# Kernel optimization log

Hardware: AMD Instinct MI355X
Metric: run time of the kernel (lower is better)

## Reference

```python
import jax, jax.numpy as jnp
import numpy as np


def setup_inputs() -> dict:
    key = jax.random.key(0)
    k1, k2, k3 = jax.random.split(key, 3)
    B, S, H, E = 4, 4096, 7168, 256
    return {
        "hidden_states": jax.random.normal(k1, (B, S, H), dtype=jnp.float32),
        "gate_weight": jax.random.normal(k2, (E, H), dtype=jnp.float32) * (H ** -0.5),
        "bias": jax.random.normal(k3, (E,), dtype=jnp.float32) * 0.01,
        "n_group": 8,
        "topk_group": 4,
        "top_k": 8,
    }


def reference(hidden_states, gate_weight, bias, n_group, topk_group, top_k):
    B, S, H = hidden_states.shape
    E = gate_weight.shape[0]
    group_size = E // n_group
    x = hidden_states.reshape(-1, H)  # [T, H]
    logits = jnp.einsum("th,eh->te", x, gate_weight)  # [T, E]
    scores = jax.nn.sigmoid(logits) + bias  # [T, E]
    scores_g = scores.reshape(-1, n_group, group_size)  # [T, G, E/G]
    group_scores = scores_g.max(axis=-1)  # [T, G]
    _, sel_groups = jax.lax.top_k(group_scores, topk_group)  # [T, topk_group]
    # group mask: 1.0 for selected groups (indices are distinct, so sum of one-hots is 0/1)
    group_mask = jax.nn.one_hot(sel_groups, n_group, dtype=scores.dtype).sum(axis=1)  # [T, G]
    masked = (scores_g * group_mask[:, :, None]).reshape(-1, E)  # [T, E]
    weights, indices = jax.lax.top_k(masked, top_k)  # [T, top_k]
    weights = weights / (weights.sum(axis=-1, keepdims=True) + 1e-6)
    return weights.reshape(B, S, -1), indices.reshape(B, S, -1)
```

## Files before the change

kernel.cpp:

```cpp
#include <hip/hip_runtime.h>


#define TTOK 16384
#define EEXP 256
#define HDIM 7168
#define BM 128
#define BK 64
#define SPLITK 2
#define KSLICE (HDIM / SPLITK)
#define NSTEP (KSLICE / BK)
#define NTHR 512
#define LDS_BYTES 163840
#define ABASE 131072
#define EPI_LDS (64 * 257 * 4)

typedef __attribute__((ext_vector_type(4))) float f32x4;
typedef __attribute__((ext_vector_type(8))) _Float16 h8;

__device__ __forceinline__ void gload_lds16(const void* g, void* l) {
  typedef const __attribute__((address_space(1))) unsigned int gu32;
  typedef __attribute__((address_space(3))) unsigned int lu32;
  __builtin_amdgcn_global_load_lds((gu32*)g, (lu32*)l, 16, 0, 0);
}

__global__ __launch_bounds__(64) void pack_w_kernel(const float* __restrict__ W,
                                                    _Float16* __restrict__ blob) {
  const int kcg = blockIdx.x;
  const int eb = blockIdx.y;
  const int lane = threadIdx.x;
  const int e = eb * 16 + (lane & 15);
  const int k0 = kcg * 32 + (lane >> 4) * 8;
  const float* src = W + (size_t)e * HDIM + k0;
  h8 hi, lo;
#pragma unroll
  for (int j = 0; j < 8; ++j) {
    float x = src[j];
    _Float16 h = (_Float16)x;
    hi[j] = h;
    lo[j] = (_Float16)((x - (float)h) * 2048.0f);
  }
  char* dst = (char*)blob + ((size_t)kcg * 32 + eb * 2) * 1024 + lane * 16;
  *(h8*)dst = hi;
  *(h8*)(dst + 1024) = lo;
}

__global__ __launch_bounds__(NTHR, 2) void gate_kernel(
    const float* __restrict__ X, const _Float16* __restrict__ Wblob,
    float* __restrict__ part) {
  extern __shared__ char smem[];

  const int bid = blockIdx.x;
  const int xcd = bid & 7;
  const int slice = xcd >> 2;
  const int tb = ((bid >> 3) << 2) | (bid & 3);
  const int tok0 = tb * BM;
  const int kbase = slice * KSLICE;
  const char* blobs = (const char*)Wblob + (size_t)slice * (KSLICE / 32) * 32768;

  const int tid = threadIdx.x;
  const int lane = tid & 63;
  const int wid = tid >> 6;
  const int wr = wid >> 2;
  const int wc = wid & 3;

  f32x4 ra[4];

  f32x4 acc1[4][4], acc2[4][4];
#pragma unroll
  for (int m = 0; m < 4; ++m)
#pragma unroll
    for (int n = 0; n < 4; ++n) {
      acc1[m][n] = (f32x4){0.f, 0.f, 0.f, 0.f};
      acc2[m][n] = (f32x4){0.f, 0.f, 0.f, 0.f};
    }

  auto LOADA = [&](int T) {
    const float* p = X + (size_t)(tok0 + (tid >> 2)) * HDIM + kbase + T * BK +
                     (tid & 3) * 16;
#pragma unroll
    for (int i = 0; i < 4; ++i) ra[i] = *(const f32x4*)(p + i * 4);
  };

  auto STAGEB = [&](int T, int buf) {
    const char* gs = blobs + (size_t)T * 65536 + lane * 16;
    char* lb = smem + buf * 65536;
#pragma unroll
    for (int i = 0; i < 8; ++i) {
      const int gb = i * 8 + wid;
      gload_lds16(gs + gb * 1024, lb + gb * 1024);
    }
  };

  auto STOREA = [&]() {
    const int row = tid >> 2, q = tid & 3;
    char* abh = smem + ABASE;
    char* abl = smem + ABASE + 16384;
#pragma unroll
    for (int c = 0; c < 2; ++c) {
      h8 hi, lo;
#pragma unroll
      for (int half = 0; half < 2; ++half) {
        const f32x4 v = (half == 0) ? ra[2 * c] : ra[2 * c + 1];
#pragma unroll
        for (int j = 0; j < 4; ++j) {
          const float x = v[j];
          const _Float16 h = (_Float16)x;
          hi[half * 4 + j] = h;
          lo[half * 4 + j] = (_Float16)((x - (float)h) * 2048.0f);
        }
      }
      const int cc = q * 2 + c;
      const int ix = row * 128 + ((cc ^ (row & 7)) << 4);
      *(h8*)(abh + ix) = hi;
      *(h8*)(abl + ix) = lo;
    }
  };

#define PHASE(S, BUF)                                                           \
  {                                                                             \
    const char* abh = smem + ABASE;                                             \
    const char* abl = smem + ABASE + 16384;                                     \
    const char* bb = smem + (BUF) * 65536;                                      \
    h8 ah[4], al[4];                                                            \
    _Pragma("unroll") for (int m = 0; m < 4; ++m) {                             \
      const int r_ = wr * 64 + m * 16 + (lane & 15);                            \
      const int c_ = ((S) * 4 + (lane >> 4)) ^ (r_ & 7);                        \
      const int ao_ = r_ * 128 + (c_ << 4);                                     \
      ah[m] = *(const h8*)(abh + ao_);                                          \
      al[m] = *(const h8*)(abl + ao_);                                          \
    }                                                                           \
    h8 bh[4], bl[4];                                                            \
    _Pragma("unroll") for (int n = 0; n < 4; ++n) {                             \
      const int bo_ = (((S) * 16 + (wc * 4 + n)) * 2) * 1024 + lane * 16;       \
      bh[n] = *(const h8*)(bb + bo_);                                           \
      bl[n] = *(const h8*)(bb + bo_ + 1024);                                    \
    }                                                                           \
    __builtin_amdgcn_s_setprio(1);                                              \
    _Pragma("unroll") for (int n = 0; n < 4; ++n)                               \
        _Pragma("unroll") for (int m = 0; m < 4; ++m) {                         \
      acc1[m][n] = __builtin_amdgcn_mfma_f32_16x16x32_f16(ah[m], bh[n], acc1[m][n], 0, 0, 0); \
      acc2[m][n] = __builtin_amdgcn_mfma_f32_16x16x32_f16(ah[m], bl[n], acc2[m][n], 0, 0, 0); \
      acc2[m][n] = __builtin_amdgcn_mfma_f32_16x16x32_f16(al[m], bh[n], acc2[m][n], 0, 0, 0); \
    }                                                                           \
    __builtin_amdgcn_s_setprio(0);                                              \
  }

  LOADA(0);
  asm volatile("" ::: "memory");
  STAGEB(0, 0);
  STOREA();
  asm volatile("s_waitcnt vmcnt(0) lgkmcnt(0)" ::: "memory");
  __builtin_amdgcn_s_barrier();

  int buf = 0;
#pragma unroll 1
  for (int T = 0; T < NSTEP; ++T) {
    const bool pf = (T + 1 < NSTEP);
    if (pf) {
      STAGEB(T + 1, buf ^ 1);
      asm volatile("" ::: "memory");
      LOADA(T + 1);
    }
    PHASE(0, buf);
    PHASE(1, buf);
    if (pf) asm volatile("s_waitcnt vmcnt(4)" ::: "memory");
    __builtin_amdgcn_s_barrier();
    if (pf) {
      STOREA();
      asm volatile("s_waitcnt lgkmcnt(0)" ::: "memory");
      __builtin_amdgcn_s_barrier();
    }
    buf ^= 1;
  }

  float* pbase = part + ((size_t)slice * TTOK + tok0) * EEXP;
#pragma unroll
  for (int m = 0; m < 4; ++m)
#pragma unroll
    for (int n = 0; n < 4; ++n) {
      const int e = wc * 64 + n * 16 + (lane & 15);
      const int t0 = wr * 64 + m * 16 + (lane >> 4) * 4;
#pragma unroll
      for (int r = 0; r < 4; ++r)
        pbase[(size_t)(t0 + r) * EEXP + e] =
            acc1[m][n][r] + acc2[m][n][r] * (1.0f / 2048.0f);
    }
}

__global__ __launch_bounds__(256) void epilogue_kernel(
    const float* __restrict__ part, const float* __restrict__ bias,
    float* __restrict__ outw, float* __restrict__ outi) {
  extern __shared__ float sc[];
  const int tid = threadIdx.x;
  const long t0 = (long)blockIdx.x * 64;

  const int e4 = (tid & 63) * 4;
  const int rsub = tid >> 6;
  const f32x4 bv = *(const f32x4*)(bias + e4);
#pragma unroll
  for (int rr = 0; rr < 16; ++rr) {
    const int row = rr * 4 + rsub;
    const f32x4 a = *(const f32x4*)(part + (t0 + row) * EEXP + e4);
    const f32x4 c = *(const f32x4*)(part + ((long)TTOK + t0 + row) * EEXP + e4);
#pragma unroll
    for (int j = 0; j < 4; ++j) {
      const float v = a[j] + c[j];
      sc[row * 257 + e4 + j] = 1.0f / (1.0f + expf(-v)) + bv[j];
    }
  }
  __syncthreads();

  if (tid < 64) {
    const float* s = sc + tid * 257;
    float gmax[8];
#pragma unroll
    for (int g = 0; g < 8; ++g) {
      float mx = -1e30f;
      for (int j = 0; j < 32; ++j) mx = fmaxf(mx, s[g * 32 + j]);
      gmax[g] = mx;
    }
    unsigned selmask = 0;
    for (int it = 0; it < 4; ++it) {
      float best = -1e30f;
      int bi = 0;
      for (int g = 0; g < 8; ++g)
        if (!((selmask >> g) & 1) && gmax[g] > best) {
          best = gmax[g];
          bi = g;
        }
      selmask |= 1u << bi;
    }
    float vals[8];
    int idx[8];
#pragma unroll
    for (int j = 0; j < 8; ++j) {
      vals[j] = -1e30f;
      idx[j] = 0;
    }
    for (int e = 0; e < 256; ++e) {
      const float v = ((selmask >> (e >> 5)) & 1) ? s[e] : 0.0f;
      if (v > vals[7]) {
        int p = 7;
        while (p > 0 && v > vals[p - 1]) {
          vals[p] = vals[p - 1];
          idx[p] = idx[p - 1];
          --p;
        }
        vals[p] = v;
        idx[p] = e;
      }
    }
    float ssum = 0.0f;
#pragma unroll
    for (int j = 0; j < 8; ++j) ssum += vals[j];
    const float den = ssum + 1e-6f;
    const long tg = t0 + tid;
#pragma unroll
    for (int j = 0; j < 8; ++j) {
      outw[tg * 8 + j] = vals[j] / den;
      outi[tg * 8 + j] = (float)idx[j];
    }
  }
}

extern "C" void kernel_launch(void* const* d_in, const int* in_sizes, int n_in,
                              void* d_out, int out_size, void* d_ws, size_t ws_size,
                              hipStream_t stream) {
  const float* X = (const float*)d_in[0];
  const float* W = (const float*)d_in[1];
  const float* bias = (const float*)d_in[2];

  _Float16* wblob = (_Float16*)d_ws;
  float* part = (float*)((char*)d_ws + (size_t)EEXP * HDIM * 4);

  float* outw = (float*)d_out;
  float* outi = outw + (size_t)TTOK * 8;

  hipFuncSetAttribute((const void*)gate_kernel,
                      hipFuncAttributeMaxDynamicSharedMemorySize, LDS_BYTES);
  hipFuncSetAttribute((const void*)epilogue_kernel,
                      hipFuncAttributeMaxDynamicSharedMemorySize, EPI_LDS);

  pack_w_kernel<<<dim3(HDIM / 32, EEXP / 16), 64, 0, stream>>>(W, wblob);
  gate_kernel<<<SPLITK * (TTOK / BM), NTHR, LDS_BYTES, stream>>>(X, wblob, part);
  epilogue_kernel<<<TTOK / 64, 256, EPI_LDS, stream>>>(part, bias, outw, outi);
}
```

Before: 290.0 us.

## Split experts across blocks, shrink K tile, double-buffer A for higher occupancy

The gate GEMM now splits the 256 experts into two halves handled by separate blocks, and the K step shrinks from 64 to 32. LDS drops to 64KB and launch bounds rise to 4 blocks per CU. The A tile is now double-buffered in LDS with a two-stage register prefetch, which removes one barrier per step, and the weight blob layout is repacked per expert half. The aim is more resident waves to hide latency, at the cost of reading the activations twice (hopefully served from the shared L2) and twice as many K iterations with less MFMA work per barrier.

```diff
diff --git a/kernel.cpp b/kernel.cpp
--- a/kernel.cpp
+++ b/kernel.cpp
@@ -5,13 +5,13 @@
 #define EEXP 256
 #define HDIM 7168
 #define BM 128
-#define BK 64
+#define BE 128
+#define BK 32
 #define SPLITK 2
 #define KSLICE (HDIM / SPLITK)
 #define NSTEP (KSLICE / BK)
 #define NTHR 512
-#define LDS_BYTES 163840
-#define ABASE 131072
+#define LDS_BYTES 65536
 #define EPI_LDS (64 * 257 * 4)
 
 typedef __attribute__((ext_vector_type(4))) float f32x4;
@@ -39,35 +39,39 @@
     hi[j] = h;
     lo[j] = (_Float16)((x - (float)h) * 2048.0f);
   }
-  char* dst = (char*)blob + ((size_t)kcg * 32 + eb * 2) * 1024 + lane * 16;
+  const int slice = kcg / NSTEP, kcl = kcg % NSTEP;
+  const int ehalf = eb >> 3, ebl = eb & 7;
+  char* dst = (char*)blob + ((size_t)(slice * 2 + ehalf) * NSTEP + kcl) * 16384 +
+              (ebl * 2) * 1024 + lane * 16;
   *(h8*)dst = hi;
   *(h8*)(dst + 1024) = lo;
 }
 
-__global__ __launch_bounds__(NTHR, 2) void gate_kernel(
+__global__ __launch_bounds__(NTHR, 4) void gate_kernel(
     const float* __restrict__ X, const _Float16* __restrict__ Wblob,
     float* __restrict__ part) {
   extern __shared__ char smem[];
 
   const int bid = blockIdx.x;
-  const int xcd = bid & 7;
-  const int slice = xcd >> 2;
-  const int tb = ((bid >> 3) << 2) | (bid & 3);
+  const int slice = (bid & 7) >> 2;
+  const int ehalf = (bid >> 3) & 1;
+  const int tb = ((bid >> 4) << 2) | (bid & 3);
   const int tok0 = tb * BM;
   const int kbase = slice * KSLICE;
-  const char* blobs = (const char*)Wblob + (size_t)slice * (KSLICE / 32) * 32768;
+  const char* blobs = (const char*)Wblob +
+                      ((size_t)(slice * 2 + ehalf) * NSTEP) * 16384;
 
   const int tid = threadIdx.x;
   const int lane = tid & 63;
   const int wid = tid >> 6;
-  const int wr = wid >> 2;
-  const int wc = wid & 3;
-
-  f32x4 ra[4];
-
-  f32x4 acc1[4][4], acc2[4][4];
-#pragma unroll
-  for (int m = 0; m < 4; ++m)
+  const int wr = wid >> 1;
+  const int wc = wid & 1;
+
+  f32x4 ra[2];
+
+  f32x4 acc1[2][4], acc2[2][4];
+#pragma unroll
+  for (int m = 0; m < 2; ++m)
 #pragma unroll
     for (int n = 0; n < 4; ++n) {
       acc1[m][n] = (f32x4){0.f, 0.f, 0.f, 0.f};
@@ -76,110 +80,99 @@
 
   auto LOADA = [&](int T) {
     const float* p = X + (size_t)(tok0 + (tid >> 2)) * HDIM + kbase + T * BK +
-                     (tid & 3) * 16;
-#pragma unroll
-    for (int i = 0; i < 4; ++i) ra[i] = *(const f32x4*)(p + i * 4);
+                     (tid & 3) * 8;
+    ra[0] = *(const f32x4*)p;
+    ra[1] = *(const f32x4*)(p + 4);
   };
 
   auto STAGEB = [&](int T, int buf) {
-    const char* gs = blobs + (size_t)T * 65536 + lane * 16;
-    char* lb = smem + buf * 65536;
-#pragma unroll
-    for (int i = 0; i < 8; ++i) {
-      const int gb = i * 8 + wid;
-      gload_lds16(gs + gb * 1024, lb + gb * 1024);
-    }
-  };
-
-  auto STOREA = [&]() {
+    const char* gs = blobs + (size_t)T * 16384 + lane * 16;
+    char* lb = smem + buf * 16384 + lane * 16;
+    gload_lds16(gs + (wid * 2) * 1024, lb + (wid * 2) * 1024);
+    gload_lds16(gs + (wid * 2 + 1) * 1024, lb + (wid * 2 + 1) * 1024);
+  };
+
+  auto STOREA = [&](int buf) {
+    h8 hi, lo;
+#pragma unroll
+    for (int half = 0; half < 2; ++half) {
+      const f32x4 v = ra[half];
+#pragma unroll
+      for (int j = 0; j < 4; ++j) {
+        const float x = v[j];
+        const _Float16 h = (_Float16)x;
+        hi[half * 4 + j] = h;
+        lo[half * 4 + j] = (_Float16)((x - (float)h) * 2048.0f);
+      }
+    }
+    char* ah = smem + 32768 + buf * 16384;
     const int row = tid >> 2, q = tid & 3;
-    char* abh = smem + ABASE;
-    char* abl = smem + ABASE + 16384;
-#pragma unroll
-    for (int c = 0; c < 2; ++c) {
-      h8 hi, lo;
-#pragma unroll
-      for (int half = 0; half < 2; ++half) {
-        const f32x4 v = (half == 0) ? ra[2 * c] : ra[2 * c + 1];
-#pragma unroll
-        for (int j = 0; j < 4; ++j) {
-          const float x = v[j];
-          const _Float16 h = (_Float16)x;
-          hi[half * 4 + j] = h;
-          lo[half * 4 + j] = (_Float16)((x - (float)h) * 2048.0f);
-        }
+    *(h8*)(ah + q * 2048 + row * 16) = hi;
+    *(h8*)(ah + 8192 + q * 2048 + row * 16) = lo;
+  };
+
+  auto PHASE = [&](int buf) {
+    const char* ahp = smem + 32768 + buf * 16384;
+    const char* bb = smem + buf * 16384;
+    h8 ah[2], al[2];
+#pragma unroll
+    for (int m = 0; m < 2; ++m) {
+      const int r_ = wr * 32 + m * 16 + (lane & 15);
+      const int ao_ = (lane >> 4) * 2048 + r_ * 16;
+      ah[m] = *(const h8*)(ahp + ao_);
+      al[m] = *(const h8*)(ahp + 8192 + ao_);
+    }
+    __builtin_amdgcn_s_setprio(1);
+#pragma unroll
+    for (int n = 0; n < 4; ++n) {
+      const int bo_ = ((wc * 4 + n) * 2) * 1024 + lane * 16;
+      const h8 bh = *(const h8*)(bb + bo_);
+      const h8 bl = *(const h8*)(bb + bo_ + 1024);
+#pragma unroll
+      for (int m = 0; m < 2; ++m) {
+        acc1[m][n] = __builtin_amdgcn_mfma_f32_16x16x32_f16(ah[m], bh, acc1[m][n], 0, 0, 0);
+        acc2[m][n] = __builtin_amdgcn_mfma_f32_16x16x32_f16(ah[m], bl, acc2[m][n], 0, 0, 0);
+        acc2[m][n] = __builtin_amdgcn_mfma_f32_16x16x32_f16(al[m], bh, acc2[m][n], 0, 0, 0);
       }
-      const int cc = q * 2 + c;
-      const int ix = row * 128 + ((cc ^ (row & 7)) << 4);
-      *(h8*)(abh + ix) = hi;
-      *(h8*)(abl + ix) = lo;
-    }
-  };
-
-#define PHASE(S, BUF)                                                           \
-  {                                                                             \
-    const char* abh = smem + ABASE;                                             \
-    const char* abl = smem + ABASE + 16384;                                     \
-    const char* bb = smem + (BUF) * 65536;                                      \
-    h8 ah[4], al[4];                                                            \
-    _Pragma("unroll") for (int m = 0; m < 4; ++m) {                             \
-      const int r_ = wr * 64 + m * 16 + (lane & 15);                            \
-      const int c_ = ((S) * 4 + (lane >> 4)) ^ (r_ & 7);                        \
-      const int ao_ = r_ * 128 + (c_ << 4);                                     \
-      ah[m] = *(const h8*)(abh + ao_);                                          \
-      al[m] = *(const h8*)(abl + ao_);                                          \
-    }                                                                           \
-    h8 bh[4], bl[4];                                                            \
-    _Pragma("unroll") for (int n = 0; n < 4; ++n) {                             \
-      const int bo_ = (((S) * 16 + (wc * 4 + n)) * 2) * 1024 + lane * 16;       \
-      bh[n] = *(const h8*)(bb + bo_);                                           \
-      bl[n] = *(const h8*)(bb + bo_ + 1024);                                    \
-    }                                                                           \
-    __builtin_amdgcn_s_setprio(1);                                              \
-    _Pragma("unroll") for (int n = 0; n < 4; ++n)                               \
-        _Pragma("unroll") for (int m = 0; m < 4; ++m) {                         \
-      acc1[m][n] = __builtin_amdgcn_mfma_f32_16x16x32_f16(ah[m], bh[n], acc1[m][n], 0, 0, 0); \
-      acc2[m][n] = __builtin_amdgcn_mfma_f32_16x16x32_f16(ah[m], bl[n], acc2[m][n], 0, 0, 0); \
-      acc2[m][n] = __builtin_amdgcn_mfma_f32_16x16x32_f16(al[m], bh[n], acc2[m][n], 0, 0, 0); \
-    }                                                                           \
-    __builtin_amdgcn_s_setprio(0);                                              \
-  }
+    }
+    __builtin_amdgcn_s_setprio(0);
+  };
 
   LOADA(0);
   asm volatile("" ::: "memory");
   STAGEB(0, 0);
-  STOREA();
-  asm volatile("s_waitcnt vmcnt(0) lgkmcnt(0)" ::: "memory");
+  asm volatile("" ::: "memory");
+  STOREA(0);
+  LOADA(1);
+  asm volatile("s_waitcnt vmcnt(2) lgkmcnt(0)" ::: "memory");
   __builtin_amdgcn_s_barrier();
 
-  int buf = 0;
+  int p = 0;
 #pragma unroll 1
   for (int T = 0; T < NSTEP; ++T) {
-    const bool pf = (T + 1 < NSTEP);
-    if (pf) {
-      STAGEB(T + 1, buf ^ 1);
+    if (T + 1 < NSTEP) {
+      STAGEB(T + 1, p ^ 1);
       asm volatile("" ::: "memory");
-      LOADA(T + 1);
-    }
-    PHASE(0, buf);
-    PHASE(1, buf);
-    if (pf) asm volatile("s_waitcnt vmcnt(4)" ::: "memory");
+      STOREA(p ^ 1);
+      if (T + 2 < NSTEP) LOADA(T + 2);
+    }
+    PHASE(p);
+    if (T + 2 < NSTEP) {
+      asm volatile("s_waitcnt vmcnt(2) lgkmcnt(0)" ::: "memory");
+    } else {
+      asm volatile("s_waitcnt vmcnt(0) lgkmcnt(0)" ::: "memory");
+    }
     __builtin_amdgcn_s_barrier();
-    if (pf) {
-      STOREA();
-      asm volatile("s_waitcnt lgkmcnt(0)" ::: "memory");
-      __builtin_amdgcn_s_barrier();
-    }
-    buf ^= 1;
-  }
-
-  float* pbase = part + ((size_t)slice * TTOK + tok0) * EEXP;
-#pragma unroll
-  for (int m = 0; m < 4; ++m)
+    p ^= 1;
+  }
+
+  float* pbase = part + ((size_t)slice * TTOK + tok0) * EEXP + ehalf * BE;
+#pragma unroll
+  for (int m = 0; m < 2; ++m)
 #pragma unroll
     for (int n = 0; n < 4; ++n) {
       const int e = wc * 64 + n * 16 + (lane & 15);
-      const int t0 = wr * 64 + m * 16 + (lane >> 4) * 4;
+      const int t0 = wr * 32 + m * 16 + (lane >> 4) * 4;
 #pragma unroll
       for (int r = 0; r < 4; ++r)
         pbase[(size_t)(t0 + r) * EEXP + e] =
@@ -282,6 +275,6 @@
                       hipFuncAttributeMaxDynamicSharedMemorySize, EPI_LDS);
 
   pack_w_kernel<<<dim3(HDIM / 32, EEXP / 16), 64, 0, stream>>>(W, wblob);
-  gate_kernel<<<SPLITK * (TTOK / BM), NTHR, LDS_BYTES, stream>>>(X, wblob, part);
+  gate_kernel<<<SPLITK * 2 * (TTOK / BM), NTHR, LDS_BYTES, stream>>>(X, wblob, part);
   epilogue_kernel<<<TTOK / 64, 256, EPI_LDS, stream>>>(part, bias, outw, outi);
 }
```

After: 299.3 us. 3.2% more time.
